# Performance work log

Hardware: AMD Instinct MI355X
Metric: run time of the kernel (lower is better)

The kernel has to match this reference:

```python
import jax, jax.numpy as jnp
import numpy as np

N_HEADS = 8
EMBED_C = 256  # key/query channels
OUT_C = 256    # value/output channels
MASK_CENTER = True

def setup_inputs() -> dict:
    key = jax.random.key(0)
    ks = jax.random.split(key, 5)
    B, C, H, W = 32, 256, 32, 32
    x = jax.random.normal(ks[0], (B, C, H, W), dtype=jnp.float32)
    # 1x1 conv weights as [out, in] matrices; scaled like torch conv default init
    s = 1.0 / np.sqrt(C)
    q_w = jax.random.normal(ks[1], (EMBED_C, C), dtype=jnp.float32) * s
    q_b = jax.random.normal(ks[2], (EMBED_C,), dtype=jnp.float32) * s
    kv_w = jax.random.normal(ks[3], (EMBED_C + OUT_C, C), dtype=jnp.float32) * s
    kv_b = jax.random.normal(ks[4], (EMBED_C + OUT_C,), dtype=jnp.float32) * s
    return {"x": x, "q_w": q_w, "q_b": q_b, "kv_w": kv_w, "kv_b": kv_b}

def _to_multihead(t):
    # t: (B, C, S) -> (B, n_heads, S, C // n_heads)
    B, C, S = t.shape
    return jnp.transpose(t.reshape(B, N_HEADS, C // N_HEADS, S), (0, 1, 3, 2))

def reference(x, q_w, q_b, kv_w, kv_b):
    B, C, H, W = x.shape
    S = H * W
    xf = x.reshape(B, C, S)  # flatten spatial; 1x1 conv == channel matmul
    q = jnp.einsum('oc,bcs->bos', q_w, xf) + q_b[None, :, None]
    kv = jnp.einsum('oc,bcs->bos', kv_w, xf) + kv_b[None, :, None]
    k, v = kv[:, :EMBED_C], kv[:, EMBED_C:]
    q = _to_multihead(q)   # (B, h, S, dk)
    k = _to_multihead(k)   # (B, h, S, dk)
    v = _to_multihead(v)   # (B, h, S, dv)
    dk = k.shape[-1]
    # strictly-lower-triangular causal mask (center pixel masked)
    mask = jnp.tril(jnp.ones((S, S), dtype=x.dtype), -int(MASK_CENTER))
    scores = jnp.einsum('bhqd,bhkd->bhqk', q, k) / jnp.sqrt(jnp.asarray(dk, x.dtype))
    scores = jnp.where(mask == 0, jnp.asarray(-10000.0, x.dtype), scores)
    attn = jax.nn.softmax(scores, axis=-1)
    attn = jnp.where(mask == 0, jnp.asarray(0.0, x.dtype), attn)
    out = jnp.einsum('bhqk,bhkd->bhqd', attn, v)  # (B, h, S, dv)
    out = jnp.transpose(out, (0, 1, 3, 2)).reshape(B, OUT_C, H, W)
    return out
```

## Files before the change

### kernel.cpp

```cpp
#include <hip/hip_runtime.h>
#include <hip/hip_bf16.h>

typedef __attribute__((ext_vector_type(8))) short short8;
typedef __attribute__((ext_vector_type(4))) float f32x4;
typedef __attribute__((ext_vector_type(16))) float f32x16;

#define B_  32
#define CH  256
#define S_  1024
#define NH  8
#define HD  32

static __device__ __forceinline__ unsigned short f2bf(float f) {
  __hip_bfloat16 h = __float2bfloat16(f);
  return *reinterpret_cast<unsigned short*>(&h);
}

static __device__ __forceinline__ void gl_lds16(const void* g, void* l) {
  __builtin_amdgcn_global_load_lds(
      (const __attribute__((address_space(1))) void*)g,
      (__attribute__((address_space(3))) void*)l, 16, 0, 0);
}

__global__ void k_prep(const float* __restrict__ x, unsigned short* __restrict__ xt,
                       const float* __restrict__ qw, const float* __restrict__ qb,
                       const float* __restrict__ kvw, const float* __restrict__ kvb,
                       unsigned short* __restrict__ wt, float* __restrict__ bias) {
  __shared__ float tile[32][33];
  int blk = (int)blockIdx.x;
  int t = threadIdx.x;
  if (blk < 8192) {
    int b = blk >> 8;
    int inner = blk & 255;
    int ct = inner >> 5, st = inner & 31;
    int c0 = ct * 32, s0 = st * 32;
    int r = t >> 3, q4 = (t & 7) * 4;
    const float4 v = *reinterpret_cast<const float4*>(
        x + ((size_t)(b * CH + c0 + r)) * S_ + s0 + q4);
    tile[r][q4 + 0] = v.x; tile[r][q4 + 1] = v.y;
    tile[r][q4 + 2] = v.z; tile[r][q4 + 3] = v.w;
    __syncthreads();
    ushort4 u;
    u.x = f2bf(tile[q4 + 0][r]); u.y = f2bf(tile[q4 + 1][r]);
    u.z = f2bf(tile[q4 + 2][r]); u.w = f2bf(tile[q4 + 3][r]);
    *reinterpret_cast<ushort4*>(xt + ((size_t)(b * S_ + s0 + r)) * CH + c0 + q4) = u;
  } else {
    int gid = (blk - 8192) * 256 + t;
    const float rs = 0.25503531838951954f;
    int o = gid >> 8, c = gid & 255;
    float v = (o < 256) ? qw[o * 256 + c] * rs : kvw[(o - 256) * 256 + c];
    wt[gid] = f2bf(v);
    if (gid < 768) bias[gid] = (gid < 256) ? qb[gid] * rs : kvb[gid - 256];
  }
}


#define VMW(n) asm volatile("s_waitcnt vmcnt(" #n ")" ::: "memory")
#define BARX() asm volatile("s_barrier" ::: "memory")

#define PROJ_ISSUE(step, buf) do {                                  \
    gl_lds16(wa + (step) * 32,      asb + (buf) * 8192 + wb);       \
    gl_lds16(wa + (step) * 32 + 16, asb + (buf) * 8192 + 4096 + wb);\
    gl_lds16(xa + (step) * 32,      bsb + (buf) * 8192 + wb);       \
    gl_lds16(xa + (step) * 32 + 16, bsb + (buf) * 8192 + 4096 + wb);\
  } while (0)

#define PROJ_COMPUTE(buf) do {                                      \
    short8 af[4], bfv[4];                                           \
    _Pragma("unroll")                                               \
    for (int mf = 0; mf < 4; ++mf)                                  \
      af[mf] = *reinterpret_cast<const short8*>(                    \
          &As[buf][rb * 1024 + (wm + mf * 16 + lr) * 8]);           \
    _Pragma("unroll")                                               \
    for (int nf = 0; nf < 4; ++nf)                                  \
      bfv[nf] = *reinterpret_cast<const short8*>(                   \
          &Bs[buf][rb * 1024 + (wn + nf * 16 + lr) * 8]);           \
    _Pragma("unroll")                                               \
    for (int mf = 0; mf < 4; ++mf)                                  \
      _Pragma("unroll")                                             \
      for (int nf = 0; nf < 4; ++nf)                                \
        acc[mf][nf] = __builtin_amdgcn_mfma_f32_16x16x32_bf16(      \
            af[mf], bfv[nf], acc[mf][nf], 0, 0, 0);                 \
  } while (0)

__global__ __launch_bounds__(256) void k_proj(
    const unsigned short* __restrict__ wt, const float* __restrict__ bias,
    const unsigned short* __restrict__ xt,
    unsigned short* __restrict__ qws, unsigned short* __restrict__ kv) {
  __shared__ __align__(16) unsigned short As[3][4096];
  __shared__ __align__(16) unsigned short Bs[3][4096];
  int b = blockIdx.y;
  int mt = blockIdx.x >> 3, nt = blockIdx.x & 7;
  int tid = threadIdx.x;
  int wid = tid >> 6, l = tid & 63;
  int rb = l >> 4, lr = l & 15;
  int wr = wid >> 1, wc = wid & 1;
  int mb = mt * 128, nb = nt * 128;
  int wm = wr * 64, wn = wc * 64;
  const unsigned short* xb = xt + (size_t)b * S_ * CH;

  int rrow = tid & 127, kb2 = tid >> 7;
  const unsigned short* wa = wt + (size_t)(mb + rrow) * CH + kb2 * 8;
  const unsigned short* xa = xb + (size_t)(nb + rrow) * CH + kb2 * 8;
  char* asb = (char*)&As[0][0];
  char* bsb = (char*)&Bs[0][0];
  int wb = wid * 1024;

  f32x4 acc[4][4];
  #pragma unroll
  for (int mf = 0; mf < 4; ++mf)
    #pragma unroll
    for (int nf = 0; nf < 4; ++nf)
      acc[mf][nf] = (f32x4){0.f, 0.f, 0.f, 0.f};

  PROJ_ISSUE(0, 0); PROJ_ISSUE(1, 1);

  VMW(4); BARX(); PROJ_ISSUE(2, 2); PROJ_COMPUTE(0);
  VMW(4); BARX(); PROJ_ISSUE(3, 0); PROJ_COMPUTE(1);
  VMW(4); BARX(); PROJ_ISSUE(4, 1); PROJ_COMPUTE(2);
  VMW(4); BARX(); PROJ_ISSUE(5, 2); PROJ_COMPUTE(0);
  VMW(4); BARX(); PROJ_ISSUE(6, 0); PROJ_COMPUTE(1);
  VMW(4); BARX(); PROJ_ISSUE(7, 1); PROJ_COMPUTE(2);
  VMW(4); BARX();                   PROJ_COMPUTE(0);
  VMW(0); BARX();                   PROJ_COMPUTE(1);

  #pragma unroll
  for (int mf = 0; mf < 4; ++mf) {
    int m0 = mb + wm + mf * 16 + rb * 4;
    const float4 bv = *reinterpret_cast<const float4*>(bias + m0);
    #pragma unroll
    for (int nf = 0; nf < 4; ++nf) {
      int n = nb + wn + nf * 16 + lr;
      float v0 = acc[mf][nf][0] + bv.x;
      float v1 = acc[mf][nf][1] + bv.y;
      float v2 = acc[mf][nf][2] + bv.z;
      float v3 = acc[mf][nf][3] + bv.w;
      if (m0 < 256) {
        int h = m0 >> 5, d = m0 & 31;
        ushort4 u = {f2bf(v0), f2bf(v1), f2bf(v2), f2bf(v3)};
        *reinterpret_cast<ushort4*>(
            qws + ((size_t)(b * NH + h) * S_ + n) * HD + d) = u;
      } else if (m0 < 512) {
        int mm = m0 - 256; int h = mm >> 5, d0 = mm & 31;
        size_t off = (((size_t)(b * NH + h) * 32 + (n >> 5)) * 2048)
                   + (size_t)((d0 >> 3) * 256 + (n & 31) * 8 + (d0 & 7));
        ushort4 u = {f2bf(v0), f2bf(v1), f2bf(v2), f2bf(v3)};
        *reinterpret_cast<ushort4*>(kv + off) = u;
      } else {
        int mm = m0 - 512; int h = mm >> 5, d0 = mm & 31;
        int nl = n & 31;
        int kp = (nl & 19) | (((nl >> 2) & 1) << 3) | (((nl >> 3) & 1) << 2);
        size_t base = (((size_t)(b * NH + h) * 32 + (n >> 5)) * 2048) + 1024
                    + (size_t)((kp >> 3) * 256 + (kp & 7));
        kv[base + (size_t)(d0 + 0) * 8] = f2bf(v0);
        kv[base + (size_t)(d0 + 1) * 8] = f2bf(v1);
        kv[base + (size_t)(d0 + 2) * 8] = f2bf(v2);
        kv[base + (size_t)(d0 + 3) * 8] = f2bf(v3);
      }
    }
  }
}

__global__ __launch_bounds__(512, 4) void k_attn(
    const unsigned short* __restrict__ qws, const unsigned short* __restrict__ kv,
    float* __restrict__ out) {
  __shared__ __align__(16) unsigned short kvbuf[2][8192];
  int tid = threadIdx.x;
  int wid = tid >> 6, l = tid & 63;
  int col = l & 31, hi = l >> 5;
  int bh = (int)(blockIdx.x & 255);
  int g  = 3 - (int)(blockIdx.x >> 8);
  int qt = g * 8 + wid;
  int q0 = qt << 5;
  int niter = g * 2 + 2;

  const unsigned short* Q   = qws + (size_t)bh * S_ * HD;
  const unsigned short* kvb = kv + (size_t)bh * 32 * 2048;
  char* kb0 = (char*)&kvbuf[0][0];
  int wb = wid * 1024;

  short8 aq0 = *reinterpret_cast<const short8*>(Q + (q0 + col) * HD + hi * 8);
  short8 aq1 = *reinterpret_cast<const short8*>(Q + (q0 + col) * HD + 16 + hi * 8);

  f32x16 z, O;
  #pragma unroll
  for (int i = 0; i < 16; ++i) { z[i] = 0.f; O[i] = 0.f; }
  float lsA = 0.f, lsB = 0.f;

  gl_lds16(kvb + tid * 8,        kb0 + wb);
  gl_lds16(kvb + 4096 + tid * 8, kb0 + 8192 + wb);
  __syncthreads();

  #pragma unroll 1
  for (int i = 0; i < niter; ++i) {
    int cur = i & 1;
    bool more = (i + 1 < niter);
    if (more) {
      const unsigned short* src = kvb + (size_t)(i + 1) * 8192 + tid * 8;
      char* dst = kb0 + (cur ^ 1) * 16384 + wb;
      gl_lds16(src,        dst);
      gl_lds16(src + 4096, dst + 8192);
    }

    #pragma unroll
    for (int sub = 0; sub < 4; ++sub) {
      int t = 4 * i + sub;
      if (qt >= t) {
        const unsigned short* Kb = &kvbuf[cur][sub * 2048];
        short8 bk0 = *reinterpret_cast<const short8*>(Kb + hi * 256 + col * 8);
        short8 bk1 = *reinterpret_cast<const short8*>(Kb + 512 + hi * 256 + col * 8);
        short8 av0 = *reinterpret_cast<const short8*>(Kb + 1024 + hi * 256 + col * 8);
        short8 av1 = *reinterpret_cast<const short8*>(Kb + 1536 + hi * 256 + col * 8);

        f32x16 st = __builtin_amdgcn_mfma_f32_32x32x16_bf16(bk0, aq0, z, 0, 0, 0);
        st = __builtin_amdgcn_mfma_f32_32x32x16_bf16(bk1, aq1, st, 0, 0, 0);

        float p[16];
        if (t == qt) {
          #pragma unroll
          for (int r = 0; r < 16; ++r) {
            int key = (r & 3) + 8 * (r >> 2) + 4 * hi;
            float e = __builtin_amdgcn_exp2f(st[r]);
            p[r] = (key < col) ? e : 0.f;
          }
        } else {
          #pragma unroll
          for (int r = 0; r < 16; ++r) p[r] = __builtin_amdgcn_exp2f(st[r]);
        }

        lsA += ((p[0] + p[1]) + (p[2] + p[3])) + ((p[4] + p[5]) + (p[6] + p[7]));
        lsB += ((p[8] + p[9]) + (p[10] + p[11])) + ((p[12] + p[13]) + (p[14] + p[15]));

        union { unsigned int u[8]; short8 v[2]; } pb;
        #pragma unroll
        for (int jj = 0; jj < 8; ++jj)
          asm("v_cvt_pk_bf16_f32 %0, %1, %2"
              : "=v"(pb.u[jj]) : "v"(p[2 * jj]), "v"(p[2 * jj + 1]));

        O = __builtin_amdgcn_mfma_f32_32x32x16_bf16(av0, pb.v[0], O, 0, 0, 0);
        O = __builtin_amdgcn_mfma_f32_32x32x16_bf16(av1, pb.v[1], O, 0, 0, 0);
      }
    }

    __syncthreads();
  }

  float lsum = lsA + lsB;
  float ltot = lsum + __shfl_xor(lsum, 32);
  float linv = (ltot > 0.f) ? 1.f / ltot : 0.f;
  int b = bh >> 3, h = bh & 7;
  float* ob = out + ((size_t)(b * 256 + h * 32)) * S_ + q0 + col;
  #pragma unroll
  for (int r = 0; r < 16; ++r) {
    int d = (r & 3) + 8 * (r >> 2) + 4 * hi;
    ob[(size_t)d * S_] = O[r] * linv;
  }
}

extern "C" void kernel_launch(void* const* d_in, const int* in_sizes, int n_in,
                              void* d_out, int out_size, void* d_ws, size_t ws_size,
                              hipStream_t stream) {
  const float* x   = (const float*)d_in[0];
  const float* qw  = (const float*)d_in[1];
  const float* qb  = (const float*)d_in[2];
  const float* kvw = (const float*)d_in[3];
  const float* kvb = (const float*)d_in[4];
  float* out = (float*)d_out;

  char* ws = (char*)d_ws;
  unsigned short* wt   = (unsigned short*)(ws + 0);
  float*          bias = (float*)(ws + 393216);
  unsigned short* xt   = (unsigned short*)(ws + 396288);
  unsigned short* qws  = (unsigned short*)(ws + 17173504);
  unsigned short* kv   = (unsigned short*)(ws + 33950720);

  k_prep<<<8960, 256, 0, stream>>>(x, xt, qw, qb, kvw, kvb, wt, bias);
  k_proj<<<dim3(48, 32), 256, 0, stream>>>(wt, bias, xt, qws, kv);
  k_attn<<<1024, 512, 0, stream>>>(qws, kv, out);
}
```

Baseline: 79.81 us.

## Load projection MFMA operands directly from global memory, dropping LDS staging

```diff
diff --git a/kernel.cpp b/kernel.cpp
--- a/kernel.cpp
+++ b/kernel.cpp
@@ -55,40 +55,30 @@
 }
 
 
-#define VMW(n) asm volatile("s_waitcnt vmcnt(" #n ")" ::: "memory")
-#define BARX() asm volatile("s_barrier" ::: "memory")
-
-#define PROJ_ISSUE(step, buf) do {                                  \
-    gl_lds16(wa + (step) * 32,      asb + (buf) * 8192 + wb);       \
-    gl_lds16(wa + (step) * 32 + 16, asb + (buf) * 8192 + 4096 + wb);\
-    gl_lds16(xa + (step) * 32,      bsb + (buf) * 8192 + wb);       \
-    gl_lds16(xa + (step) * 32 + 16, bsb + (buf) * 8192 + 4096 + wb);\
-  } while (0)
-
-#define PROJ_COMPUTE(buf) do {                                      \
-    short8 af[4], bfv[4];                                           \
+#define LDF(P, step) do {                                           \
     _Pragma("unroll")                                               \
     for (int mf = 0; mf < 4; ++mf)                                  \
-      af[mf] = *reinterpret_cast<const short8*>(                    \
-          &As[buf][rb * 1024 + (wm + mf * 16 + lr) * 8]);           \
+      P##a[mf] = *reinterpret_cast<const short8*>(                  \
+          wA + mf * 16 * CH + (step) * 32);                         \
     _Pragma("unroll")                                               \
     for (int nf = 0; nf < 4; ++nf)                                  \
-      bfv[nf] = *reinterpret_cast<const short8*>(                   \
-          &Bs[buf][rb * 1024 + (wn + nf * 16 + lr) * 8]);           \
+      P##b[nf] = *reinterpret_cast<const short8*>(                  \
+          xB + nf * 16 * CH + (step) * 32);                         \
+  } while (0)
+
+#define CMP(P) do {                                                 \
     _Pragma("unroll")                                               \
     for (int mf = 0; mf < 4; ++mf)                                  \
       _Pragma("unroll")                                             \
       for (int nf = 0; nf < 4; ++nf)                                \
         acc[mf][nf] = __builtin_amdgcn_mfma_f32_16x16x32_bf16(      \
-            af[mf], bfv[nf], acc[mf][nf], 0, 0, 0);                 \
+            P##a[mf], P##b[nf], acc[mf][nf], 0, 0, 0);              \
   } while (0)
 
 __global__ __launch_bounds__(256) void k_proj(
     const unsigned short* __restrict__ wt, const float* __restrict__ bias,
     const unsigned short* __restrict__ xt,
     unsigned short* __restrict__ qws, unsigned short* __restrict__ kv) {
-  __shared__ __align__(16) unsigned short As[3][4096];
-  __shared__ __align__(16) unsigned short Bs[3][4096];
   int b = blockIdx.y;
   int mt = blockIdx.x >> 3, nt = blockIdx.x & 7;
   int tid = threadIdx.x;
@@ -97,14 +87,10 @@
   int wr = wid >> 1, wc = wid & 1;
   int mb = mt * 128, nb = nt * 128;
   int wm = wr * 64, wn = wc * 64;
-  const unsigned short* xb = xt + (size_t)b * S_ * CH;
-
-  int rrow = tid & 127, kb2 = tid >> 7;
-  const unsigned short* wa = wt + (size_t)(mb + rrow) * CH + kb2 * 8;
-  const unsigned short* xa = xb + (size_t)(nb + rrow) * CH + kb2 * 8;
-  char* asb = (char*)&As[0][0];
-  char* bsb = (char*)&Bs[0][0];
-  int wb = wid * 1024;
+
+  const unsigned short* wA = wt + (size_t)(mb + wm + lr) * CH + rb * 8;
+  const unsigned short* xB = xt + (size_t)b * S_ * CH
+                           + (size_t)(nb + wn + lr) * CH + rb * 8;
 
   f32x4 acc[4][4];
   #pragma unroll
@@ -113,16 +99,17 @@
     for (int nf = 0; nf < 4; ++nf)
       acc[mf][nf] = (f32x4){0.f, 0.f, 0.f, 0.f};
 
-  PROJ_ISSUE(0, 0); PROJ_ISSUE(1, 1);
-
-  VMW(4); BARX(); PROJ_ISSUE(2, 2); PROJ_COMPUTE(0);
-  VMW(4); BARX(); PROJ_ISSUE(3, 0); PROJ_COMPUTE(1);
-  VMW(4); BARX(); PROJ_ISSUE(4, 1); PROJ_COMPUTE(2);
-  VMW(4); BARX(); PROJ_ISSUE(5, 2); PROJ_COMPUTE(0);
-  VMW(4); BARX(); PROJ_ISSUE(6, 0); PROJ_COMPUTE(1);
-  VMW(4); BARX(); PROJ_ISSUE(7, 1); PROJ_COMPUTE(2);
-  VMW(4); BARX();                   PROJ_COMPUTE(0);
-  VMW(0); BARX();                   PROJ_COMPUTE(1);
+  short8 Pa[4], Pb[4], Qa[4], Qb[4];
+
+  LDF(P, 0); LDF(Q, 1);
+  CMP(P); LDF(P, 2);
+  CMP(Q); LDF(Q, 3);
+  CMP(P); LDF(P, 4);
+  CMP(Q); LDF(Q, 5);
+  CMP(P); LDF(P, 6);
+  CMP(Q); LDF(Q, 7);
+  CMP(P);
+  CMP(Q);
 
   #pragma unroll
   for (int mf = 0; mf < 4; ++mf) {
```

Result: slower. 97.05 us (+21.6%).
